# Performance work log

Hardware: AMD Instinct MI355X
Metric: run time of the kernel (lower is better)

Reference implementation:

```python
import jax, jax.numpy as jnp
import numpy as np

HID = 128

def setup_inputs() -> dict:
    key = jax.random.key(0)
    ks = jax.random.split(key, 16)
    T, N, E = 32, 10000, 160000
    features = jax.random.normal(ks[0], (T, N, 1), dtype=jnp.float32)
    src = jax.random.randint(ks[1], (E,), 0, N)
    dst = jax.random.randint(ks[2], (E,), 0, N)
    s = 0.1
    # GraphConv params (stored as [in,out] so y = x @ W + b)
    W1 = jax.random.normal(ks[3], (1, 32), dtype=jnp.float32) * s
    b1 = jnp.zeros((32,), jnp.float32)
    W2 = jax.random.normal(ks[4], (32, HID), dtype=jnp.float32) * s
    b2 = jnp.zeros((HID,), jnp.float32)
    # attention-pool gate nn.Linear(128,1)
    gate_w = jax.random.normal(ks[5], (HID, 1), dtype=jnp.float32) * s
    gate_b = jnp.zeros((1,), jnp.float32)
    # GRU params, PyTorch layout: [3H, in], gate order (r, z, n)
    W_ih = jax.random.normal(ks[6], (3 * HID, HID), dtype=jnp.float32) * s
    W_hh = jax.random.normal(ks[7], (3 * HID, HID), dtype=jnp.float32) * s
    b_ih = jnp.zeros((3 * HID,), jnp.float32)
    b_hh = jnp.zeros((3 * HID,), jnp.float32)
    # dense layers ([in,out])
    d1_w = jax.random.normal(ks[8], (HID, 16), dtype=jnp.float32) * s
    d1_b = jnp.zeros((16,), jnp.float32)
    d2_w = jax.random.normal(ks[9], (16, 4), dtype=jnp.float32) * s
    d2_b = jnp.zeros((4,), jnp.float32)
    return {"features": features, "src": src, "dst": dst,
            "W1": W1, "b1": b1, "W2": W2, "b2": b2,
            "gate_w": gate_w, "gate_b": gate_b,
            "W_ih": W_ih, "W_hh": W_hh, "b_ih": b_ih, "b_hh": b_hh,
            "d1_w": d1_w, "d1_b": d1_b, "d2_w": d2_w, "d2_b": d2_b}


def reference(features, src, dst, W1, b1, W2, b2, gate_w, gate_b,
              W_ih, W_hh, b_ih, b_hh, d1_w, d1_b, d2_w, d2_b):
    T, N, _ = features.shape
    E = src.shape[0]
    ones = jnp.ones((E,), features.dtype)
    out_deg = jnp.clip(jax.ops.segment_sum(ones, src, num_segments=N), 1.0)
    in_deg = jnp.clip(jax.ops.segment_sum(ones, dst, num_segments=N), 1.0)
    norm_out = out_deg ** -0.5  # DGL GraphConv norm='both' (src side)
    norm_in = in_deg ** -0.5    # dst side

    def gconv(h, W, b):
        # h: [N, F] -> scale by src norm, gather, scatter-add to dst, scale, linear, SiLU
        msg = (h * norm_out[:, None])[src]               # [E, F]
        agg = jax.ops.segment_sum(msg, dst, num_segments=N)  # [N, F]
        return jax.nn.silu((agg * norm_in[:, None]) @ W + b)

    def per_frame(f):  # f: [N,1]
        return gconv(gconv(f, W1, b1), W2, b2)  # [N, HID]

    h = jax.vmap(per_frame)(features)  # [T, N, HID]

    # GlobalAttentionPooling: softmax over nodes of gate_nn(h)
    gate = h @ gate_w + gate_b                 # [T, N, 1]
    alpha = jax.nn.softmax(gate, axis=1)
    pooled = jnp.sum(alpha * h, axis=1)        # [T, HID]

    # single-layer GRU, batch=1, take final hidden state
    def gru_step(hprev, x):
        gi = x @ W_ih.T + b_ih
        gh = hprev @ W_hh.T + b_hh
        i_r, i_z, i_n = jnp.split(gi, 3)
        h_r, h_z, h_n = jnp.split(gh, 3)
        r = jax.nn.sigmoid(i_r + h_r)
        z = jax.nn.sigmoid(i_z + h_z)
        n = jnp.tanh(i_n + r * h_n)
        hnew = (1.0 - z) * n + z * hprev
        return hnew, None

    h0 = jnp.zeros((HID,), features.dtype)
    hT, _ = jax.lax.scan(gru_step, h0, pooled)

    out = jax.nn.silu(hT @ d1_w + d1_b)
    out = jax.nn.silu(out @ d2_w + d2_b)
    return jax.nn.sigmoid(out).reshape(1, 4)
```

## Files before the change

### kernel.cpp

```cpp
#include <hip/hip_runtime.h>
#include <stdint.h>

#define T_FRAMES 32
#define NNODES 10000
#define NEDGES 160000
#define HID 128
#define GXL 157

#define H1_SCALE 512.0f
#define H1_INV   (1.0f/512.0f)

typedef short v8s __attribute__((ext_vector_type(8)));
typedef float v4f __attribute__((ext_vector_type(4)));

static __device__ __forceinline__ ushort f2bf(float f){
  uint32_t u = __float_as_uint(f);
  u += 0x7FFFu + ((u >> 16) & 1u);
  return (ushort)(u >> 16);
}
static __device__ __forceinline__ float fsigm(float x){
  return __fdividef(1.0f, 1.0f + __expf(-x));
}
static __device__ __forceinline__ float fsilu(float x){
  return x * fsigm(x);
}
static __device__ __forceinline__ float ftanh(float x){
  return 2.0f * fsigm(2.0f * x) - 1.0f;
}


__global__ void k_degree(const int* __restrict__ src, const int* __restrict__ dst,
                         int* cnt_out, int* cnt_in, int E){
  int e = blockIdx.x*blockDim.x + threadIdx.x;
  if (e < E){
    atomicAdd(&cnt_out[src[e]], 1);
    atomicAdd(&cnt_in[dst[e]], 1);
  }
}

__global__ void __launch_bounds__(1024) k_scan(const int* __restrict__ cnt_in,
                                               const int* __restrict__ cnt_out,
                                               int* row_ptr, int* cursor,
                                               float* norm_out, float* norm_in, int N){
  __shared__ int wsum[16];
  __shared__ int wexcl[16];
  int tid = threadIdx.x, lane = tid & 63, wid = tid >> 6;
  const int C = 10;
  int base = tid * C;
  int v[C];
  int s = 0;
  #pragma unroll
  for (int i = 0; i < C; ++i){
    int idx = base + i;
    int c = (idx < N) ? cnt_in[idx] : 0;
    v[i] = c;
    s += c;
    if (idx < N){
      norm_in[idx]  = rsqrtf((float)max(c, 1));
      norm_out[idx] = rsqrtf((float)max(cnt_out[idx], 1));
    }
  }
  int x = s;
  #pragma unroll
  for (int off = 1; off < 64; off <<= 1){
    int y = __shfl_up(x, off);
    if (lane >= off) x += y;
  }
  if (lane == 63) wsum[wid] = x;
  __syncthreads();
  if (tid == 0){
    int run = 0;
    #pragma unroll
    for (int w = 0; w < 16; ++w){ int t = wsum[w]; wexcl[w] = run; run += t; }
    row_ptr[N] = run;
  }
  __syncthreads();
  int run = wexcl[wid] + x - s;
  #pragma unroll
  for (int i = 0; i < C; ++i){
    int idx = base + i;
    if (idx < N){ row_ptr[idx] = run; cursor[idx] = run; run += v[i]; }
  }
}

__global__ void k_fill(const int* __restrict__ src, const int* __restrict__ dst,
                       int* cursor, int* es, int E){
  int e = blockIdx.x*blockDim.x + threadIdx.x;
  if (e < E){
    int p = atomicAdd(&cursor[dst[e]], 1);
    es[p] = src[e];
  }
}


__global__ void __launch_bounds__(256) k_fnT(const float* __restrict__ feat,
                                             const float* __restrict__ norm_o,
                                             float* __restrict__ fnT,
                                             const float* __restrict__ W2,
                                             ushort* __restrict__ W2F, int N){
  __shared__ float sm[32][65];
  int n0 = blockIdx.x*64;
  int tid = threadIdx.x;
  for (int idx = tid; idx < 2048; idx += 256){
    int t = idx >> 6, i = idx & 63;
    int n = n0 + i;
    sm[t][i] = (n < N) ? feat[(size_t)t*N + n] : 0.f;
  }
  __syncthreads();
  for (int idx = tid; idx < 2048; idx += 256){
    int i = idx >> 5, t = idx & 31;
    int n = n0 + i;
    if (n < N) fnT[(size_t)n*32 + t] = sm[t][i] * norm_o[n];
  }
  if (blockIdx.x < 16){
    int t2 = blockIdx.x*256 + tid;
    int j = t2 & 7, l = (t2 >> 3) & 63, i = t2 >> 9;
    int g = l >> 4, n = l & 15;
    W2F[t2] = f2bf(W2[(g*8 + j)*128 + i*16 + n]);
  }
}


__global__ void __launch_bounds__(256) k_gconv1_nm(
    const float* __restrict__ fnT, const int* __restrict__ row_ptr,
    const int* __restrict__ es, const float* __restrict__ norm_in,
    const float* __restrict__ norm_out,
    const float* __restrict__ W1, const float* __restrict__ b1,
    uchar* __restrict__ h1s, int N){
  __shared__ float w1s[32], b1s[32];
  int tid = threadIdx.x;
  if (tid < 32){ w1s[tid] = W1[tid]; b1s[tid] = b1[tid]; }
  __syncthreads();
  int n = blockIdx.x*4 + (tid >> 6);
  int lane = tid & 63;
  int ep = lane >> 5, t = lane & 31;
  int s = row_ptr[n], d = row_ptr[n+1];
  float acc = 0.f;
  int e = s + ep;
  for (; e + 6 < d; e += 8){
    float v0 = fnT[(size_t)es[e]  *32 + t];
    float v1 = fnT[(size_t)es[e+2]*32 + t];
    float v2 = fnT[(size_t)es[e+4]*32 + t];
    float v3 = fnT[(size_t)es[e+6]*32 + t];
    acc += v0 + v1 + v2 + v3;
  }
  for (; e < d; e += 2)
    acc += fnT[(size_t)es[e]*32 + t];
  acc += __shfl_xor(acc, 32);
  float x1 = acc * norm_in[n];
  float x1p = __shfl(x1, lane >> 1);
  float no = norm_out[n];
  int j0 = (lane & 1) * 16;
  float hv[16];
  #pragma unroll
  for (int q = 0; q < 16; ++q)
    hv[q] = fsilu(fmaf(x1p, w1s[j0+q], b1s[j0+q])) * no;
  uint b[4] = {0u, 0u, 0u, 0u};
  #pragma unroll
  for (int q = 0; q < 16; ++q){
    float t8 = fminf(fmaxf(fmaf(hv[q], H1_SCALE, 128.5f), 0.f), 255.f);
    b[q >> 2] |= ((uint)(int)t8) << ((q & 3) * 8);
  }
  *(uint4*)(h1s + (size_t)n*1024 + lane*16) = make_uint4(b[0], b[1], b[2], b[3]);
}


__global__ void __launch_bounds__(256) k_gconv2_nm(
    const uchar* __restrict__ h1s, const int* __restrict__ row_ptr,
    const int* __restrict__ es, const float* __restrict__ norm_in,
    ushort* __restrict__ x2F, int N){
  int tid = threadIdx.x;
  int n = blockIdx.x*4 + (tid >> 6);
  int lane = tid & 63;
  int s = row_ptr[n], d = row_ptr[n+1];
  float acc[16];
  #pragma unroll
  for (int i = 0; i < 16; ++i) acc[i] = 0.f;

  #define ACCB(v) do { \
    acc[0]  += (float)((v).x & 0xffu);         acc[1]  += (float)(((v).x >> 8) & 0xffu); \
    acc[2]  += (float)(((v).x >> 16) & 0xffu); acc[3]  += (float)((v).x >> 24); \
    acc[4]  += (float)((v).y & 0xffu);         acc[5]  += (float)(((v).y >> 8) & 0xffu); \
    acc[6]  += (float)(((v).y >> 16) & 0xffu); acc[7]  += (float)((v).y >> 24); \
    acc[8]  += (float)((v).z & 0xffu);         acc[9]  += (float)(((v).z >> 8) & 0xffu); \
    acc[10] += (float)(((v).z >> 16) & 0xffu); acc[11] += (float)((v).z >> 24); \
    acc[12] += (float)((v).w & 0xffu);         acc[13] += (float)(((v).w >> 8) & 0xffu); \
    acc[14] += (float)(((v).w >> 16) & 0xffu); acc[15] += (float)((v).w >> 24); \
  } while(0)

  int e = s;
  for (; e + 7 < d; e += 8){
    uint4 w0 = *((const uint4*)(h1s + (size_t)es[e]  *1024) + lane);
    uint4 w1 = *((const uint4*)(h1s + (size_t)es[e+1]*1024) + lane);
    uint4 w2 = *((const uint4*)(h1s + (size_t)es[e+2]*1024) + lane);
    uint4 w3 = *((const uint4*)(h1s + (size_t)es[e+3]*1024) + lane);
    uint4 w4 = *((const uint4*)(h1s + (size_t)es[e+4]*1024) + lane);
    uint4 w5 = *((const uint4*)(h1s + (size_t)es[e+5]*1024) + lane);
    uint4 w6 = *((const uint4*)(h1s + (size_t)es[e+6]*1024) + lane);
    uint4 w7 = *((const uint4*)(h1s + (size_t)es[e+7]*1024) + lane);
    ACCB(w0); ACCB(w1); ACCB(w2); ACCB(w3);
    ACCB(w4); ACCB(w5); ACCB(w6); ACCB(w7);
  }
  for (; e < d; ++e){
    uint4 w0 = *((const uint4*)(h1s + (size_t)es[e]*1024) + lane);
    ACCB(w0);
  }
  #undef ACCB

  float ni = norm_in[n];
  float corr = -128.0f * (float)(d - s);
  float sc = H1_INV * ni;
  uint w[8];
  #pragma unroll
  for (int q = 0; q < 8; ++q){
    float v0 = (acc[2*q]   + corr) * sc;
    float v1 = (acc[2*q+1] + corr) * sc;
    w[q] = (uint)f2bf(v0) | ((uint)f2bf(v1) << 16);
  }
  ushort* dp = x2F + (size_t)(lane >> 1)*N*32 + (size_t)n*32 + (lane & 1)*16;
  *(uint4*)dp       = make_uint4(w[0], w[1], w[2], w[3]);
  *((uint4*)dp + 1) = make_uint4(w[4], w[5], w[6], w[7]);
}


__global__ void __launch_bounds__(256) k_linear_fused(
    const ushort* __restrict__ x2F, const ushort* __restrict__ W2F,
    const float* __restrict__ b2, const float* __restrict__ gate_w,
    const float* __restrict__ gate_b,
    float* __restrict__ Zp, float* __restrict__ pooled_un, int N){
  __shared__ float pool_s[128];
  __shared__ float z_s[4];
  int t = blockIdx.y;
  int tid = threadIdx.x;
  int wave = tid >> 6, lane = tid & 63;
  int g = lane >> 4, n = lane & 15;
  if (tid < 128) pool_s[tid] = 0.f;
  if (tid < 4) z_s[tid] = 0.f;
  __syncthreads();
  int tile = blockIdx.x*4 + wave;
  bool active = (tile*16 < N);

  const v8s* W2Fv = (const v8s*)W2F;
  v8s bfrag[8];
  #pragma unroll
  for (int i = 0; i < 8; ++i) bfrag[i] = W2Fv[i*64 + lane];
  v4f acc[8];
  #pragma unroll
  for (int i = 0; i < 8; ++i){
    float bv = b2[i*16 + n];
    acc[i] = (v4f){bv, bv, bv, bv};
  }
  if (active){
    int nb = tile*16;
    const v8s* ap = (const v8s*)(x2F + (size_t)t*N*32 + (size_t)nb*32);
    v8s a = ap[n*4 + g];
    #pragma unroll
    for (int i = 0; i < 8; ++i)
      acc[i] = __builtin_amdgcn_mfma_f32_16x16x32_bf16(a, bfrag[i], acc[i], 0, 0, 0);

    float hs[8][4];
    #pragma unroll
    for (int i = 0; i < 8; ++i){
      #pragma unroll
      for (int r = 0; r < 4; ++r) hs[i][r] = fsilu(acc[i][r]);
    }
    float gw8[8];
    #pragma unroll
    for (int i = 0; i < 8; ++i) gw8[i] = gate_w[i*16 + n];
    float gp[4] = {0.f, 0.f, 0.f, 0.f};
    #pragma unroll
    for (int i = 0; i < 8; ++i){
      #pragma unroll
      for (int r = 0; r < 4; ++r) gp[r] += hs[i][r] * gw8[i];
    }
    #pragma unroll
    for (int m = 1; m < 16; m <<= 1){
      #pragma unroll
      for (int r = 0; r < 4; ++r) gp[r] += __shfl_xor(gp[r], m);
    }
    float gb = gate_b[0];
    float wn[4];
    #pragma unroll
    for (int r = 0; r < 4; ++r) wn[r] = __expf(gp[r] + gb);

    float se = (n == 0) ? (wn[0] + wn[1] + wn[2] + wn[3]) : 0.f;
    se += __shfl_xor(se, 16);
    se += __shfl_xor(se, 32);
    if (lane == 0) z_s[wave] = se;

    float cs[8];
    #pragma unroll
    for (int i = 0; i < 8; ++i){
      float c = 0.f;
      #pragma unroll
      for (int r = 0; r < 4; ++r) c += hs[i][r] * wn[r];
      c += __shfl_xor(c, 16);
      c += __shfl_xor(c, 32);
      cs[i] = c;
    }
    if (lane < 16){
      #pragma unroll
      for (int i = 0; i < 8; ++i) atomicAdd(&pool_s[i*16 + lane], cs[i]);
    }
  }
  __syncthreads();
  if (tid == 0)
    Zp[(size_t)t*GXL + blockIdx.x] = z_s[0] + z_s[1] + z_s[2] + z_s[3];
  if (tid < 128) atomicAdd(&pooled_un[(size_t)t*HID + tid], pool_s[tid]);
}


__global__ void __launch_bounds__(384) k_gi(const float* __restrict__ pooled_un,
                                            const float* __restrict__ Zp,
                                            const float* __restrict__ W_ih,
                                            const float* __restrict__ b_ih,
                                            float* __restrict__ gi_all){
  __shared__ float ps[HID];
  __shared__ float zred[6];
  int t = blockIdx.x, tid = threadIdx.x;
  int lane = tid & 63, wid = tid >> 6;
  float zs = 0.f;
  for (int i = tid; i < GXL; i += 384) zs += Zp[(size_t)t*GXL + i];
  #pragma unroll
  for (int m = 32; m; m >>= 1) zs += __shfl_xor(zs, m);
  if (lane == 0) zred[wid] = zs;
  __syncthreads();
  float invZ = __fdividef(1.0f, zred[0]+zred[1]+zred[2]+zred[3]+zred[4]+zred[5]);
  if (tid < HID) ps[tid] = pooled_un[(size_t)t*HID + tid] * invZ;
  __syncthreads();
  float acc = b_ih[tid];
  const float4* wr = (const float4*)(W_ih + (size_t)tid*HID);
  const float4* p4 = (const float4*)ps;
  #pragma unroll
  for (int q = 0; q < HID/4; ++q){
    float4 wv = wr[q], pv = p4[q];
    acc = fmaf(wv.x, pv.x, acc);
    acc = fmaf(wv.y, pv.y, acc);
    acc = fmaf(wv.z, pv.z, acc);
    acc = fmaf(wv.w, pv.w, acc);
  }
  gi_all[t*384 + tid] = acc;
}

__global__ void __launch_bounds__(768) k_gru(
    const float* __restrict__ gi_all, const float* __restrict__ W_hh,
    const float* __restrict__ b_hh,
    const float* __restrict__ d1_w, const float* __restrict__ d1_b,
    const float* __restrict__ d2_w, const float* __restrict__ d2_b,
    float* __restrict__ out){
  __shared__ float gi_s[T_FRAMES*3*HID];
  __shared__ float ps[2*384];
  __shared__ float h_s[HID];
  __shared__ float o1[16];
  int tid = threadIdx.x;
  int half = (tid >= 384) ? 1 : 0;
  int o = tid - half*384;

  for (int i = tid; i < T_FRAMES*3*HID; i += 768) gi_s[i] = gi_all[i];

  const float4* wr = (const float4*)(W_hh + (size_t)o*HID + half*64);
  #define LDW(i) float4 W##i = wr[i];
  LDW(0) LDW(1) LDW(2) LDW(3) LDW(4) LDW(5) LDW(6) LDW(7)
  LDW(8) LDW(9) LDW(10) LDW(11) LDW(12) LDW(13) LDW(14) LDW(15)
  #undef LDW
  float bh2 = half ? 0.f : b_hh[o];

  if (tid < HID) h_s[tid] = 0.f;
  __syncthreads();

  for (int t = 0; t < T_FRAMES; ++t){
    const float4* p4 = (const float4*)h_s + half*16;
    float acc = bh2;
    #define STEP(i) { float4 pv = p4[i]; \
      acc = fmaf(W##i.x, pv.x, acc); acc = fmaf(W##i.y, pv.y, acc); \
      acc = fmaf(W##i.z, pv.z, acc); acc = fmaf(W##i.w, pv.w, acc); }
    STEP(0) STEP(1) STEP(2) STEP(3) STEP(4) STEP(5) STEP(6) STEP(7)
    STEP(8) STEP(9) STEP(10) STEP(11) STEP(12) STEP(13) STEP(14) STEP(15)
    #undef STEP
    ps[tid] = acc;
    __syncthreads();
    if (tid < HID){
      const float* gi = gi_s + t*384;
      float ghr = ps[tid]       + ps[384+tid];
      float ghz = ps[128+tid]   + ps[512+tid];
      float ghn = ps[256+tid]   + ps[640+tid];
      float r  = fsigm(gi[tid]       + ghr);
      float z  = fsigm(gi[HID+tid]   + ghz);
      float nn = ftanh(gi[2*HID+tid] + r*ghn);
      h_s[tid] = (1.f - z)*nn + z*h_s[tid];
    }
    __syncthreads();
  }
  if (tid < 16){
    float acc = d1_b[tid];
    #pragma unroll 4
    for (int j = 0; j < HID; ++j) acc = fmaf(h_s[j], d1_w[j*16 + tid], acc);
    o1[tid] = fsilu(acc);
  }
  __syncthreads();
  if (tid < 4){
    float acc = d2_b[tid];
    #pragma unroll
    for (int j = 0; j < 16; ++j) acc = fmaf(o1[j], d2_w[j*4 + tid], acc);
    out[tid] = fsigm(fsilu(acc));
  }
}


extern "C" void kernel_launch(void* const* d_in, const int* in_sizes, int n_in,
                              void* d_out, int out_size, void* d_ws, size_t ws_size,
                              hipStream_t stream){
  const float* features = (const float*)d_in[0];
  const int*   src      = (const int*)  d_in[1];
  const int*   dst      = (const int*)  d_in[2];
  const float* W1       = (const float*)d_in[3];
  const float* b1       = (const float*)d_in[4];
  const float* W2       = (const float*)d_in[5];
  const float* b2       = (const float*)d_in[6];
  const float* gate_w   = (const float*)d_in[7];
  const float* gate_b   = (const float*)d_in[8];
  const float* W_ih     = (const float*)d_in[9];
  const float* W_hh     = (const float*)d_in[10];
  const float* b_ih     = (const float*)d_in[11];
  const float* b_hh     = (const float*)d_in[12];
  const float* d1_w     = (const float*)d_in[13];
  const float* d1_b     = (const float*)d_in[14];
  const float* d2_w     = (const float*)d_in[15];
  const float* d2_b     = (const float*)d_in[16];
  float* out = (float*)d_out;

  const int N = NNODES, E = NEDGES, T = T_FRAMES;

  char* base = (char*)d_ws;
  size_t off = 0;
  auto alloc = [&](size_t bytes)->void*{
    void* p = base + off;
    off = (off + bytes + 255) & ~(size_t)255;
    return p;
  };
  int*    cnt_out = (int*)   alloc((size_t)N*4);
  int*    cnt_in  = (int*)   alloc((size_t)N*4);
  float*  pooled  = (float*) alloc((size_t)T*HID*4);
  size_t zero_span = off;
  int*    row_ptr = (int*)   alloc((size_t)(N+1)*4);
  int*    cursor  = (int*)   alloc((size_t)N*4);
  float*  norm_o  = (float*) alloc((size_t)N*4);
  float*  norm_i  = (float*) alloc((size_t)N*4);
  int*    es      = (int*)   alloc((size_t)E*4);
  float*  fnT     = (float*) alloc((size_t)N*T*4);
  uchar*  h1s     = (uchar*) alloc((size_t)N*1024);
  ushort* x2F     = (ushort*)alloc((size_t)T*N*32*2);
  float*  Zp      = (float*) alloc((size_t)T*GXL*4);
  float*  gi_all  = (float*) alloc((size_t)T*3*HID*4);
  ushort* W2F     = (ushort*)alloc((size_t)8*64*8*2);
  (void)ws_size; (void)in_sizes; (void)n_in; (void)out_size;

  hipMemsetAsync(d_ws, 0, zero_span, stream);

  k_degree<<<(E+255)/256, 256, 0, stream>>>(src, dst, cnt_out, cnt_in, E);
  k_scan  <<<1, 1024, 0, stream>>>(cnt_in, cnt_out, row_ptr, cursor, norm_o, norm_i, N);
  k_fill  <<<(E+255)/256, 256, 0, stream>>>(src, dst, cursor, es, E);

  k_fnT      <<<(N+63)/64, 256, 0, stream>>>(features, norm_o, fnT, W2, W2F, N);
  k_gconv1_nm<<<N/4, 256, 0, stream>>>(fnT, row_ptr, es, norm_i, norm_o, W1, b1, h1s, N);
  k_gconv2_nm<<<N/4, 256, 0, stream>>>(h1s, row_ptr, es, norm_i, x2F, N);

  k_linear_fused<<<dim3(GXL, T), 256, 0, stream>>>(x2F, W2F, b2, gate_w, gate_b, Zp, pooled, N);

  k_gi <<<T, 384, 0, stream>>>(pooled, Zp, W_ih, b_ih, gi_all);
  k_gru<<<1, 768, 0, stream>>>(gi_all, W_hh, b_hh, d1_w, d1_b, d2_w, d2_b, out);
}
```

Measured before the change: 178.4 us.

## Store gconv2 output node-major and replace pooled atomics with per-block partials

The gconv2 output moves from a frame-major scattered layout to a contiguous node-major layout, so each wave writes 2KB in one contiguous run instead of many strided 32-byte pieces. The linear kernel now reads its 64-byte A-fragments from per-node rows. The global atomicAdd into pooled is replaced by per-block partial sums, which k_gi reduces with three thread groups, and pooled is dropped from the zeroed span. This trades some extra partial-buffer traffic and reduction work in k_gi for removing atomic contention and scattered writes.

```diff
diff --git a/kernel.cpp b/kernel.cpp
--- a/kernel.cpp
+++ b/kernel.cpp
@@ -168,7 +168,7 @@
 __global__ void __launch_bounds__(256) k_gconv2_nm(
     const uchar* __restrict__ h1s, const int* __restrict__ row_ptr,
     const int* __restrict__ es, const float* __restrict__ norm_in,
-    ushort* __restrict__ x2F, int N){
+    ushort* __restrict__ x2, int N){
   int tid = threadIdx.x;
   int n = blockIdx.x*4 + (tid >> 6);
   int lane = tid & 63;
@@ -217,17 +217,17 @@
     float v1 = (acc[2*q+1] + corr) * sc;
     w[q] = (uint)f2bf(v0) | ((uint)f2bf(v1) << 16);
   }
-  ushort* dp = x2F + (size_t)(lane >> 1)*N*32 + (size_t)n*32 + (lane & 1)*16;
-  *(uint4*)dp       = make_uint4(w[0], w[1], w[2], w[3]);
-  *((uint4*)dp + 1) = make_uint4(w[4], w[5], w[6], w[7]);
+  uint4* dp = (uint4*)(x2 + (size_t)n*1024 + lane*16);
+  dp[0] = make_uint4(w[0], w[1], w[2], w[3]);
+  dp[1] = make_uint4(w[4], w[5], w[6], w[7]);
 }
 
 
 __global__ void __launch_bounds__(256) k_linear_fused(
-    const ushort* __restrict__ x2F, const ushort* __restrict__ W2F,
+    const ushort* __restrict__ x2, const ushort* __restrict__ W2F,
     const float* __restrict__ b2, const float* __restrict__ gate_w,
     const float* __restrict__ gate_b,
-    float* __restrict__ Zp, float* __restrict__ pooled_un, int N){
+    float* __restrict__ Zp, float* __restrict__ pool_part, int N){
   __shared__ float pool_s[128];
   __shared__ float z_s[4];
   int t = blockIdx.y;
@@ -252,8 +252,8 @@
   }
   if (active){
     int nb = tile*16;
-    const v8s* ap = (const v8s*)(x2F + (size_t)t*N*32 + (size_t)nb*32);
-    v8s a = ap[n*4 + g];
+    const v8s* ap = (const v8s*)(x2 + (size_t)(nb + (lane & 15))*1024 + t*32);
+    v8s a = ap[g];
     #pragma unroll
     for (int i = 0; i < 8; ++i)
       acc[i] = __builtin_amdgcn_mfma_f32_16x16x32_bf16(a, bfrag[i], acc[i], 0, 0, 0);
@@ -306,27 +306,35 @@
   __syncthreads();
   if (tid == 0)
     Zp[(size_t)t*GXL + blockIdx.x] = z_s[0] + z_s[1] + z_s[2] + z_s[3];
-  if (tid < 128) atomicAdd(&pooled_un[(size_t)t*HID + tid], pool_s[tid]);
-}
-
-
-__global__ void __launch_bounds__(384) k_gi(const float* __restrict__ pooled_un,
+  if (tid < 128)
+    pool_part[((size_t)t*GXL + blockIdx.x)*HID + tid] = pool_s[tid];
+}
+
+
+__global__ void __launch_bounds__(384) k_gi(const float* __restrict__ pool_part,
                                             const float* __restrict__ Zp,
                                             const float* __restrict__ W_ih,
                                             const float* __restrict__ b_ih,
                                             float* __restrict__ gi_all){
   __shared__ float ps[HID];
+  __shared__ float pp[3][HID];
   __shared__ float zred[6];
   int t = blockIdx.x, tid = threadIdx.x;
   int lane = tid & 63, wid = tid >> 6;
   float zs = 0.f;
-  for (int i = tid; i < GXL; i += 384) zs += Zp[(size_t)t*GXL + i];
+  for (int b = tid; b < GXL; b += 384) zs += Zp[(size_t)t*GXL + b];
   #pragma unroll
   for (int m = 32; m; m >>= 1) zs += __shfl_xor(zs, m);
   if (lane == 0) zred[wid] = zs;
+  int grp = tid >> 7;
+  int c = tid & 127;
+  float ss = 0.f;
+  for (int b = grp; b < GXL; b += 3)
+    ss += pool_part[((size_t)t*GXL + b)*HID + c];
+  pp[grp][c] = ss;
   __syncthreads();
   float invZ = __fdividef(1.0f, zred[0]+zred[1]+zred[2]+zred[3]+zred[4]+zred[5]);
-  if (tid < HID) ps[tid] = pooled_un[(size_t)t*HID + tid] * invZ;
+  if (tid < HID) ps[tid] = (pp[0][tid] + pp[1][tid] + pp[2][tid]) * invZ;
   __syncthreads();
   float acc = b_ih[tid];
   const float4* wr = (const float4*)(W_ih + (size_t)tid*HID);
@@ -438,21 +446,21 @@
     off = (off + bytes + 255) & ~(size_t)255;
     return p;
   };
-  int*    cnt_out = (int*)   alloc((size_t)N*4);
-  int*    cnt_in  = (int*)   alloc((size_t)N*4);
-  float*  pooled  = (float*) alloc((size_t)T*HID*4);
+  int*    cnt_out  = (int*)   alloc((size_t)N*4);
+  int*    cnt_in   = (int*)   alloc((size_t)N*4);
   size_t zero_span = off;
-  int*    row_ptr = (int*)   alloc((size_t)(N+1)*4);
-  int*    cursor  = (int*)   alloc((size_t)N*4);
-  float*  norm_o  = (float*) alloc((size_t)N*4);
-  float*  norm_i  = (float*) alloc((size_t)N*4);
-  int*    es      = (int*)   alloc((size_t)E*4);
-  float*  fnT     = (float*) alloc((size_t)N*T*4);
-  uchar*  h1s     = (uchar*) alloc((size_t)N*1024);
-  ushort* x2F     = (ushort*)alloc((size_t)T*N*32*2);
-  float*  Zp      = (float*) alloc((size_t)T*GXL*4);
-  float*  gi_all  = (float*) alloc((size_t)T*3*HID*4);
-  ushort* W2F     = (ushort*)alloc((size_t)8*64*8*2);
+  int*    row_ptr  = (int*)   alloc((size_t)(N+1)*4);
+  int*    cursor   = (int*)   alloc((size_t)N*4);
+  float*  norm_o   = (float*) alloc((size_t)N*4);
+  float*  norm_i   = (float*) alloc((size_t)N*4);
+  int*    es       = (int*)   alloc((size_t)E*4);
+  float*  fnT      = (float*) alloc((size_t)N*T*4);
+  uchar*  h1s      = (uchar*) alloc((size_t)N*1024);
+  ushort* x2       = (ushort*)alloc((size_t)N*T*32*2);
+  float*  Zp       = (float*) alloc((size_t)T*GXL*4);
+  float*  pool_part= (float*) alloc((size_t)T*GXL*HID*4);
+  float*  gi_all   = (float*) alloc((size_t)T*3*HID*4);
+  ushort* W2F      = (ushort*)alloc((size_t)8*64*8*2);
   (void)ws_size; (void)in_sizes; (void)n_in; (void)out_size;
 
   hipMemsetAsync(d_ws, 0, zero_span, stream);
@@ -463,10 +471,10 @@
 
   k_fnT      <<<(N+63)/64, 256, 0, stream>>>(features, norm_o, fnT, W2, W2F, N);
   k_gconv1_nm<<<N/4, 256, 0, stream>>>(fnT, row_ptr, es, norm_i, norm_o, W1, b1, h1s, N);
-  k_gconv2_nm<<<N/4, 256, 0, stream>>>(h1s, row_ptr, es, norm_i, x2F, N);
-
-  k_linear_fused<<<dim3(GXL, T), 256, 0, stream>>>(x2F, W2F, b2, gate_w, gate_b, Zp, pooled, N);
-
-  k_gi <<<T, 384, 0, stream>>>(pooled, Zp, W_ih, b_ih, gi_all);
+  k_gconv2_nm<<<N/4, 256, 0, stream>>>(h1s, row_ptr, es, norm_i, x2, N);
+
+  k_linear_fused<<<dim3(GXL, T), 256, 0, stream>>>(x2, W2F, b2, gate_w, gate_b, Zp, pool_part, N);
+
+  k_gi <<<T, 384, 0, stream>>>(pool_part, Zp, W_ih, b_ih, gi_all);
   k_gru<<<1, 768, 0, stream>>>(gi_all, W_hh, b_hh, d1_w, d1_b, d2_w, d2_b, out);
 }
```

Measured after the change: 186.3 us. 1.04x slower.

## Store x2 node-major and loop tiles per wave with register accumulation

Applied to the files above, without the earlier changes.

gconv2 now writes its bf16 output node-major, so each lane's store is one contiguous 64-byte chunk per node instead of being spread across frame planes. The linear/pool kernel shrinks from 157 to 32 blocks per frame. Each wave loops over several 16-node tiles and keeps the weighted pool sums and softmax denominators in registers, reducing across lanes once at the end instead of per tile. This trades coalesced writes in gconv2 for strided 64-byte reads in the linear kernel, and runs fewer, longer blocks.

```diff
diff --git a/kernel.cpp b/kernel.cpp
--- a/kernel.cpp
+++ b/kernel.cpp
@@ -5,7 +5,7 @@
 #define NNODES 10000
 #define NEDGES 160000
 #define HID 128
-#define GXL 157
+#define LGX 32
 
 #define H1_SCALE 512.0f
 #define H1_INV   (1.0f/512.0f)
@@ -168,7 +168,7 @@
 __global__ void __launch_bounds__(256) k_gconv2_nm(
     const uchar* __restrict__ h1s, const int* __restrict__ row_ptr,
     const int* __restrict__ es, const float* __restrict__ norm_in,
-    ushort* __restrict__ x2F, int N){
+    ushort* __restrict__ x2, int N){
   int tid = threadIdx.x;
   int n = blockIdx.x*4 + (tid >> 6);
   int lane = tid & 63;
@@ -217,14 +217,14 @@
     float v1 = (acc[2*q+1] + corr) * sc;
     w[q] = (uint)f2bf(v0) | ((uint)f2bf(v1) << 16);
   }
-  ushort* dp = x2F + (size_t)(lane >> 1)*N*32 + (size_t)n*32 + (lane & 1)*16;
-  *(uint4*)dp       = make_uint4(w[0], w[1], w[2], w[3]);
-  *((uint4*)dp + 1) = make_uint4(w[4], w[5], w[6], w[7]);
+  uint4* dp = (uint4*)(x2 + (size_t)n*1024 + lane*16);
+  dp[0] = make_uint4(w[0], w[1], w[2], w[3]);
+  dp[1] = make_uint4(w[4], w[5], w[6], w[7]);
 }
 
 
 __global__ void __launch_bounds__(256) k_linear_fused(
-    const ushort* __restrict__ x2F, const ushort* __restrict__ W2F,
+    const ushort* __restrict__ x2, const ushort* __restrict__ W2F,
     const float* __restrict__ b2, const float* __restrict__ gate_w,
     const float* __restrict__ gate_b,
     float* __restrict__ Zp, float* __restrict__ pooled_un, int N){
@@ -237,23 +237,29 @@
   if (tid < 128) pool_s[tid] = 0.f;
   if (tid < 4) z_s[tid] = 0.f;
   __syncthreads();
-  int tile = blockIdx.x*4 + wave;
-  bool active = (tile*16 < N);
 
   const v8s* W2Fv = (const v8s*)W2F;
   v8s bfrag[8];
   #pragma unroll
   for (int i = 0; i < 8; ++i) bfrag[i] = W2Fv[i*64 + lane];
-  v4f acc[8];
-  #pragma unroll
-  for (int i = 0; i < 8; ++i){
-    float bv = b2[i*16 + n];
-    acc[i] = (v4f){bv, bv, bv, bv};
-  }
-  if (active){
+  float gw8[8], bv8[8];
+  #pragma unroll
+  for (int i = 0; i < 8; ++i){ gw8[i] = gate_w[i*16 + n]; bv8[i] = b2[i*16 + n]; }
+  float gb = gate_b[0];
+
+  float cs_acc[8];
+  #pragma unroll
+  for (int i = 0; i < 8; ++i) cs_acc[i] = 0.f;
+  float z_acc = 0.f;
+
+  int wslot = blockIdx.x*4 + wave;
+  for (int tile = wslot; tile*16 < N; tile += 128){
     int nb = tile*16;
-    const v8s* ap = (const v8s*)(x2F + (size_t)t*N*32 + (size_t)nb*32);
-    v8s a = ap[n*4 + g];
+    const v8s* ap = (const v8s*)(x2 + (size_t)(nb + n)*1024 + t*32);
+    v8s a = ap[g];
+    v4f acc[8];
+    #pragma unroll
+    for (int i = 0; i < 8; ++i) acc[i] = (v4f){bv8[i], bv8[i], bv8[i], bv8[i]};
     #pragma unroll
     for (int i = 0; i < 8; ++i)
       acc[i] = __builtin_amdgcn_mfma_f32_16x16x32_bf16(a, bfrag[i], acc[i], 0, 0, 0);
@@ -264,9 +270,6 @@
       #pragma unroll
       for (int r = 0; r < 4; ++r) hs[i][r] = fsilu(acc[i][r]);
     }
-    float gw8[8];
-    #pragma unroll
-    for (int i = 0; i < 8; ++i) gw8[i] = gate_w[i*16 + n];
     float gp[4] = {0.f, 0.f, 0.f, 0.f};
     #pragma unroll
     for (int i = 0; i < 8; ++i){
@@ -278,34 +281,32 @@
       #pragma unroll
       for (int r = 0; r < 4; ++r) gp[r] += __shfl_xor(gp[r], m);
     }
-    float gb = gate_b[0];
     float wn[4];
     #pragma unroll
     for (int r = 0; r < 4; ++r) wn[r] = __expf(gp[r] + gb);
-
-    float se = (n == 0) ? (wn[0] + wn[1] + wn[2] + wn[3]) : 0.f;
-    se += __shfl_xor(se, 16);
-    se += __shfl_xor(se, 32);
-    if (lane == 0) z_s[wave] = se;
-
-    float cs[8];
+    if (n == 0) z_acc += wn[0] + wn[1] + wn[2] + wn[3];
     #pragma unroll
     for (int i = 0; i < 8; ++i){
-      float c = 0.f;
       #pragma unroll
-      for (int r = 0; r < 4; ++r) c += hs[i][r] * wn[r];
-      c += __shfl_xor(c, 16);
-      c += __shfl_xor(c, 32);
-      cs[i] = c;
-    }
-    if (lane < 16){
-      #pragma unroll
-      for (int i = 0; i < 8; ++i) atomicAdd(&pool_s[i*16 + lane], cs[i]);
-    }
+      for (int r = 0; r < 4; ++r) cs_acc[i] += hs[i][r] * wn[r];
+    }
+  }
+
+  z_acc += __shfl_xor(z_acc, 16);
+  z_acc += __shfl_xor(z_acc, 32);
+  if (lane == 0) z_s[wave] = z_acc;
+  #pragma unroll
+  for (int i = 0; i < 8; ++i){
+    cs_acc[i] += __shfl_xor(cs_acc[i], 16);
+    cs_acc[i] += __shfl_xor(cs_acc[i], 32);
+  }
+  if (lane < 16){
+    #pragma unroll
+    for (int i = 0; i < 8; ++i) atomicAdd(&pool_s[i*16 + lane], cs_acc[i]);
   }
   __syncthreads();
   if (tid == 0)
-    Zp[(size_t)t*GXL + blockIdx.x] = z_s[0] + z_s[1] + z_s[2] + z_s[3];
+    Zp[(size_t)t*LGX + blockIdx.x] = z_s[0] + z_s[1] + z_s[2] + z_s[3];
   if (tid < 128) atomicAdd(&pooled_un[(size_t)t*HID + tid], pool_s[tid]);
 }
 
@@ -320,7 +321,7 @@
   int t = blockIdx.x, tid = threadIdx.x;
   int lane = tid & 63, wid = tid >> 6;
   float zs = 0.f;
-  for (int i = tid; i < GXL; i += 384) zs += Zp[(size_t)t*GXL + i];
+  for (int i = tid; i < LGX; i += 384) zs += Zp[(size_t)t*LGX + i];
   #pragma unroll
   for (int m = 32; m; m >>= 1) zs += __shfl_xor(zs, m);
   if (lane == 0) zred[wid] = zs;
@@ -449,8 +450,8 @@
   int*    es      = (int*)   alloc((size_t)E*4);
   float*  fnT     = (float*) alloc((size_t)N*T*4);
   uchar*  h1s     = (uchar*) alloc((size_t)N*1024);
-  ushort* x2F     = (ushort*)alloc((size_t)T*N*32*2);
-  float*  Zp      = (float*) alloc((size_t)T*GXL*4);
+  ushort* x2      = (ushort*)alloc((size_t)N*T*32*2);
+  float*  Zp      = (float*) alloc((size_t)T*LGX*4);
   float*  gi_all  = (float*) alloc((size_t)T*3*HID*4);
   ushort* W2F     = (ushort*)alloc((size_t)8*64*8*2);
   (void)ws_size; (void)in_sizes; (void)n_in; (void)out_size;
@@ -463,9 +464,9 @@
 
   k_fnT      <<<(N+63)/64, 256, 0, stream>>>(features, norm_o, fnT, W2, W2F, N);
   k_gconv1_nm<<<N/4, 256, 0, stream>>>(fnT, row_ptr, es, norm_i, norm_o, W1, b1, h1s, N);
-  k_gconv2_nm<<<N/4, 256, 0, stream>>>(h1s, row_ptr, es, norm_i, x2F, N);
-
-  k_linear_fused<<<dim3(GXL, T), 256, 0, stream>>>(x2F, W2F, b2, gate_w, gate_b, Zp, pooled, N);
+  k_gconv2_nm<<<N/4, 256, 0, stream>>>(h1s, row_ptr, es, norm_i, x2, N);
+
+  k_linear_fused<<<dim3(LGX, T), 256, 0, stream>>>(x2, W2F, b2, gate_w, gate_b, Zp, pooled, N);
 
   k_gi <<<T, 384, 0, stream>>>(pooled, Zp, W_ih, b_ih, gi_all);
   k_gru<<<1, 768, 0, stream>>>(gi_all, W_hh, b_hh, d1_w, d1_b, d2_w, d2_b, out);
```

Result: no change. 178.2 us (-0.1%).

## Fuse edge fill with feature transpose, node-major x2 layout, kernel zeroing

Applied to the files above, without the earlier changes.

Merges the CSR fill kernel and the feature-transpose/W2 bf16 packing kernel into one launch, with disjoint block ranges doing each job. Changes the gconv2 output layout from frame-major scattered 32-byte stores to contiguous 2 KB rows per node, so each wave writes whole rows. The MFMA linear kernel now reads 64-byte strided slices per node. It also replaces hipMemsetAsync with a small zeroing kernel, trading a runtime memset for one more launch.

```diff
diff --git a/kernel.cpp b/kernel.cpp
--- a/kernel.cpp
+++ b/kernel.cpp
@@ -26,6 +26,12 @@
 }
 static __device__ __forceinline__ float ftanh(float x){
   return 2.0f * fsigm(2.0f * x) - 1.0f;
+}
+
+
+__global__ void k_zero(float4* __restrict__ p, int n4){
+  int i = blockIdx.x*blockDim.x + threadIdx.x;
+  if (i < n4) p[i] = make_float4(0.f, 0.f, 0.f, 0.f);
 }
 
 
@@ -83,37 +89,38 @@
   }
 }
 
-__global__ void k_fill(const int* __restrict__ src, const int* __restrict__ dst,
-                       int* cursor, int* es, int E){
-  int e = blockIdx.x*blockDim.x + threadIdx.x;
+
+__global__ void __launch_bounds__(256) k_fill_fnT(
+    const int* __restrict__ src, const int* __restrict__ dst,
+    int* cursor, int* es, int E,
+    const float* __restrict__ feat, const float* __restrict__ norm_o,
+    float* __restrict__ fnT,
+    const float* __restrict__ W2, ushort* __restrict__ W2F, int N){
+  __shared__ float sm[32][65];
+  int tid = threadIdx.x;
+  int bx = blockIdx.x;
+
+  int e = bx*256 + tid;
   if (e < E){
     int p = atomicAdd(&cursor[dst[e]], 1);
     es[p] = src[e];
   }
-}
-
-
-__global__ void __launch_bounds__(256) k_fnT(const float* __restrict__ feat,
-                                             const float* __restrict__ norm_o,
-                                             float* __restrict__ fnT,
-                                             const float* __restrict__ W2,
-                                             ushort* __restrict__ W2F, int N){
-  __shared__ float sm[32][65];
-  int n0 = blockIdx.x*64;
-  int tid = threadIdx.x;
-  for (int idx = tid; idx < 2048; idx += 256){
-    int t = idx >> 6, i = idx & 63;
-    int n = n0 + i;
-    sm[t][i] = (n < N) ? feat[(size_t)t*N + n] : 0.f;
-  }
-  __syncthreads();
-  for (int idx = tid; idx < 2048; idx += 256){
-    int i = idx >> 5, t = idx & 31;
-    int n = n0 + i;
-    if (n < N) fnT[(size_t)n*32 + t] = sm[t][i] * norm_o[n];
-  }
-  if (blockIdx.x < 16){
-    int t2 = blockIdx.x*256 + tid;
+
+  if (bx < 157){
+    int n0 = bx*64;
+    for (int idx = tid; idx < 2048; idx += 256){
+      int t = idx >> 6, i = idx & 63;
+      int n = n0 + i;
+      sm[t][i] = (n < N) ? feat[(size_t)t*N + n] : 0.f;
+    }
+    __syncthreads();
+    for (int idx = tid; idx < 2048; idx += 256){
+      int i = idx >> 5, t = idx & 31;
+      int n = n0 + i;
+      if (n < N) fnT[(size_t)n*32 + t] = sm[t][i] * norm_o[n];
+    }
+  } else if (bx < 173){
+    int t2 = (bx - 157)*256 + tid;
     int j = t2 & 7, l = (t2 >> 3) & 63, i = t2 >> 9;
     int g = l >> 4, n = l & 15;
     W2F[t2] = f2bf(W2[(g*8 + j)*128 + i*16 + n]);
@@ -168,7 +175,7 @@
 __global__ void __launch_bounds__(256) k_gconv2_nm(
     const uchar* __restrict__ h1s, const int* __restrict__ row_ptr,
     const int* __restrict__ es, const float* __restrict__ norm_in,
-    ushort* __restrict__ x2F, int N){
+    ushort* __restrict__ x2, int N){
   int tid = threadIdx.x;
   int n = blockIdx.x*4 + (tid >> 6);
   int lane = tid & 63;
@@ -217,14 +224,14 @@
     float v1 = (acc[2*q+1] + corr) * sc;
     w[q] = (uint)f2bf(v0) | ((uint)f2bf(v1) << 16);
   }
-  ushort* dp = x2F + (size_t)(lane >> 1)*N*32 + (size_t)n*32 + (lane & 1)*16;
-  *(uint4*)dp       = make_uint4(w[0], w[1], w[2], w[3]);
-  *((uint4*)dp + 1) = make_uint4(w[4], w[5], w[6], w[7]);
+  uint4* dp = (uint4*)(x2 + (size_t)n*1024 + lane*16);
+  dp[0] = make_uint4(w[0], w[1], w[2], w[3]);
+  dp[1] = make_uint4(w[4], w[5], w[6], w[7]);
 }
 
 
 __global__ void __launch_bounds__(256) k_linear_fused(
-    const ushort* __restrict__ x2F, const ushort* __restrict__ W2F,
+    const ushort* __restrict__ x2, const ushort* __restrict__ W2F,
     const float* __restrict__ b2, const float* __restrict__ gate_w,
     const float* __restrict__ gate_b,
     float* __restrict__ Zp, float* __restrict__ pooled_un, int N){
@@ -252,8 +259,8 @@
   }
   if (active){
     int nb = tile*16;
-    const v8s* ap = (const v8s*)(x2F + (size_t)t*N*32 + (size_t)nb*32);
-    v8s a = ap[n*4 + g];
+    const v8s* ap = (const v8s*)(x2 + (size_t)(nb + (lane & 15))*1024 + t*32);
+    v8s a = ap[g];
     #pragma unroll
     for (int i = 0; i < 8; ++i)
       acc[i] = __builtin_amdgcn_mfma_f32_16x16x32_bf16(a, bfrag[i], acc[i], 0, 0, 0);
@@ -449,23 +456,24 @@
   int*    es      = (int*)   alloc((size_t)E*4);
   float*  fnT     = (float*) alloc((size_t)N*T*4);
   uchar*  h1s     = (uchar*) alloc((size_t)N*1024);
-  ushort* x2F     = (ushort*)alloc((size_t)T*N*32*2);
+  ushort* x2      = (ushort*)alloc((size_t)N*T*32*2);
   float*  Zp      = (float*) alloc((size_t)T*GXL*4);
   float*  gi_all  = (float*) alloc((size_t)T*3*HID*4);
   ushort* W2F     = (ushort*)alloc((size_t)8*64*8*2);
   (void)ws_size; (void)in_sizes; (void)n_in; (void)out_size;
 
-  hipMemsetAsync(d_ws, 0, zero_span, stream);
+  int n4 = (int)(zero_span / 16);
+  k_zero  <<<(n4+255)/256, 256, 0, stream>>>((float4*)d_ws, n4);
 
   k_degree<<<(E+255)/256, 256, 0, stream>>>(src, dst, cnt_out, cnt_in, E);
   k_scan  <<<1, 1024, 0, stream>>>(cnt_in, cnt_out, row_ptr, cursor, norm_o, norm_i, N);
-  k_fill  <<<(E+255)/256, 256, 0, stream>>>(src, dst, cursor, es, E);
-
-  k_fnT      <<<(N+63)/64, 256, 0, stream>>>(features, norm_o, fnT, W2, W2F, N);
+  k_fill_fnT<<<(E+255)/256, 256, 0, stream>>>(src, dst, cursor, es, E,
+                                              features, norm_o, fnT, W2, W2F, N);
+
   k_gconv1_nm<<<N/4, 256, 0, stream>>>(fnT, row_ptr, es, norm_i, norm_o, W1, b1, h1s, N);
-  k_gconv2_nm<<<N/4, 256, 0, stream>>>(h1s, row_ptr, es, norm_i, x2F, N);
-
-  k_linear_fused<<<dim3(GXL, T), 256, 0, stream>>>(x2F, W2F, b2, gate_w, gate_b, Zp, pooled, N);
+  k_gconv2_nm<<<N/4, 256, 0, stream>>>(h1s, row_ptr, es, norm_i, x2, N);
+
+  k_linear_fused<<<dim3(GXL, T), 256, 0, stream>>>(x2, W2F, b2, gate_w, gate_b, Zp, pooled, N);
 
   k_gi <<<T, 384, 0, stream>>>(pooled, Zp, W_ih, b_ih, gi_all);
   k_gru<<<1, 768, 0, stream>>>(gi_all, W_hh, b_hh, d1_w, d1_b, d2_w, d2_b, out);
```

Result: no change. 175.3 us (median of 2 runs) (-1.7%).
